# Kernel tuning notes

Measured on AMD Instinct MI355X. Metric: run time of the kernel, lower is better.

The kernel has to match this reference:

```python
import jax, jax.numpy as jnp
import numpy as np

N_AST, M, C, D, H, OUT = 200000, 400000, 25000, 256, 4, 256


def setup_inputs() -> dict:
    key = jax.random.key(0)
    ks = jax.random.split(key, 12)
    s = 0.02
    return {
        "ast_nodes_encodings": jax.random.normal(ks[0], (N_AST, D), jnp.float32),
        "ast_node_idx_to_pdg_node_idx_mapping_key": jax.random.randint(ks[1], (M,), 0, N_AST),
        "ast_node_idx_to_pdg_node_idx_mapping_value": jax.random.randint(ks[2], (M,), 0, C),
        "pdg_node_idx_to_sub_ast_root_idx_mapping_key": jax.random.randint(ks[3], (C,), 0, C),
        "pdg_node_idx_to_sub_ast_root_idx_mapping_value": jax.random.randint(ks[4], (C,), 0, N_AST),
        "nr_cfg_nodes": C,
        "Wq": jax.random.normal(ks[5], (D, D), jnp.float32) * s,
        "bq": jnp.zeros((D,), jnp.float32),
        "Wk": jax.random.normal(ks[6], (D, D), jnp.float32) * s,
        "bk": jnp.zeros((D,), jnp.float32),
        "Wv": jax.random.normal(ks[7], (D, D), jnp.float32) * s,
        "bv": jnp.zeros((D,), jnp.float32),
        "Wo": jax.random.normal(ks[8], (D, OUT), jnp.float32) * s,
        "bo": jnp.zeros((OUT,), jnp.float32),
    }


def _scatter_attn(x, attn_keys, seg, num_segments, Wq, bq, Wk, bk, Wv, bv, Wo, bo):
    # x: [M, D] scattered inputs; attn_keys: [C, D] per-segment queries; seg: [M] segment ids.
    d_h = D // H
    q = (attn_keys @ Wq + bq).reshape(num_segments, H, d_h)  # [C,H,dh]
    k = (x @ Wk + bk).reshape(-1, H, d_h)                    # [M,H,dh]
    v = (x @ Wv + bv).reshape(-1, H, d_h)                    # [M,H,dh]
    scale = 1.0 / jnp.sqrt(jnp.asarray(d_h, x.dtype))
    scores = jnp.einsum('mhd,mhd->mh', k, q[seg]) * scale    # [M,H]
    m = jax.ops.segment_max(scores, seg, num_segments=num_segments)  # [C,H]
    e = jnp.exp(scores - m[seg])                             # [M,H]
    denom = jax.ops.segment_sum(e, seg, num_segments=num_segments)  # [C,H]
    num = jax.ops.segment_sum((e[..., None] * v).reshape(-1, H * d_h),
                              seg, num_segments=num_segments)        # [C,D]
    pooled = (num.reshape(num_segments, H, d_h) / (denom[..., None] + 1e-9)).reshape(num_segments, D)
    return pooled @ Wo + bo                                  # [C,OUT]


def reference(ast_nodes_encodings,
              ast_node_idx_to_pdg_node_idx_mapping_key,
              ast_node_idx_to_pdg_node_idx_mapping_value,
              pdg_node_idx_to_sub_ast_root_idx_mapping_key,
              pdg_node_idx_to_sub_ast_root_idx_mapping_value,
              nr_cfg_nodes, Wq, bq, Wk, bk, Wv, bv, Wo, bo):
    # Build per-CFG-node attention keys: gather sub-AST-root encodings, scatter by PDG node idx.
    root_enc = ast_nodes_encodings[pdg_node_idx_to_sub_ast_root_idx_mapping_value]  # [C,D]
    attn_keys = jnp.zeros((nr_cfg_nodes, D), ast_nodes_encodings.dtype)
    attn_keys = attn_keys.at[pdg_node_idx_to_sub_ast_root_idx_mapping_key].set(root_enc)
    # Gather AST node encodings per mapping entry and attention-pool per CFG node.
    scattered = ast_nodes_encodings[ast_node_idx_to_pdg_node_idx_mapping_key]       # [M,D]
    return _scatter_attn(scattered, attn_keys, ast_node_idx_to_pdg_node_idx_mapping_value,
                         nr_cfg_nodes, Wq, bq, Wk, bk, Wv, bv, Wo, bo)
```

## Files before the change

kernel.cpp:

```cpp
#include <hip/hip_runtime.h>
#include <hip/hip_bf16.h>
#include <math.h>

#define D 256
#define H 4
#define DH 64
#define NOUT 256

typedef short bf16x8 __attribute__((ext_vector_type(8)));
typedef float f32x4 __attribute__((ext_vector_type(4)));

__device__ __forceinline__ ushort f2bf(float f){
  uint b = __float_as_uint(f);
  b += 0x7FFF + ((b >> 16) & 1);
  return (ushort)(b >> 16);
}
__device__ __forceinline__ float bf2f(ushort u){
  return __uint_as_float(((uint)u) << 16);
}

__global__ void winner_kernel(const int* __restrict__ key, int* __restrict__ winner, int C){
  int i = blockIdx.x*256 + threadIdx.x;
  if (i < C){ int t = key[i]; if (t >= 0 && t < C) atomicMax(&winner[t], i); }
}

__global__ void count_kernel(const int* __restrict__ seg, int* __restrict__ counts, int M, int C){
  int i = blockIdx.x*256 + threadIdx.x;
  if (i < M){ int s = seg[i]; if (s >= 0 && s < C) atomicAdd(&counts[s], 1); }
}

__global__ __launch_bounds__(1024) void scan_kernel(const int* __restrict__ counts,
    int* __restrict__ offsets, int* __restrict__ pos, int C){
  __shared__ int wtot[16];
  __shared__ int wexcl[16];
  __shared__ int ctot;
  __shared__ int carry_s;
  int tid = threadIdx.x, lane = tid & 63, wave = tid >> 6;
  if (tid == 0) carry_s = 0;
  __syncthreads();
  for (int base = 0; base < C; base += 1024){
    int i = base + tid;
    int v = (i < C) ? counts[i] : 0;
    int x = v;
    #pragma unroll
    for (int d2 = 1; d2 < 64; d2 <<= 1){
      int t = __shfl_up(x, d2, 64);
      if (lane >= d2) x += t;
    }
    if (lane == 63) wtot[wave] = x;
    __syncthreads();
    if (wave == 0 && lane < 16){
      int t = wtot[lane]; int y = t;
      #pragma unroll
      for (int d2 = 1; d2 < 16; d2 <<= 1){
        int u = __shfl_up(y, d2, 64);
        if (lane >= d2) y += u;
      }
      wexcl[lane] = y - t;
      if (lane == 15) ctot = y;
    }
    __syncthreads();
    int carry = carry_s;
    int excl = carry + wexcl[wave] + x - v;
    if (i < C){ offsets[i] = excl; pos[i] = excl; }
    __syncthreads();
    if (tid == 0) carry_s = carry + ctot;
    __syncthreads();
  }
  if (tid == 0) offsets[C] = carry_s;
}

__global__ void fill_kernel(const int* __restrict__ seg, int* __restrict__ pos,
                            int* __restrict__ members, int M, int C){
  int i = blockIdx.x*256 + threadIdx.x;
  if (i < M){ int s = seg[i]; if (s >= 0 && s < C){ int p = atomicAdd(&pos[s], 1); members[p] = i; } }
}

__global__ void conv_w(const float* __restrict__ Wq, const float* __restrict__ Wk,
                       const float* __restrict__ Wv, const float* __restrict__ Wo,
                       ushort* __restrict__ WqT, ushort* __restrict__ Wk16,
                       ushort* __restrict__ WvT, ushort* __restrict__ WoT){
  int id = blockIdx.x*256 + threadIdx.x;
  int r = id >> 8, c = id & 255;
  WqT[id]  = f2bf(Wq[c*256 + r]);
  WvT[id]  = f2bf(Wv[c*256 + r]);
  WoT[id]  = f2bf(Wo[c*256 + r]);
  Wk16[id] = f2bf(Wk[id]);
}

__global__ void gather_ag(const float* __restrict__ enc, const int* __restrict__ rootval,
                          const int* __restrict__ winner, ushort* __restrict__ Ag, int C){
  int id = blockIdx.x*256 + threadIdx.x;
  if (id < C*64){
    int c = id >> 6, g = id & 63;
    int w = winner[c];
    float4 v = make_float4(0.f, 0.f, 0.f, 0.f);
    if (w >= 0) v = *(const float4*)(enc + (size_t)rootval[w]*D + g*4);
    ushort4 u; u.x = f2bf(v.x); u.y = f2bf(v.y); u.z = f2bf(v.z); u.w = f2bf(v.w);
    *(ushort4*)(Ag + (size_t)c*D + g*4) = u;
  }
}

template<bool OUT_BF16>
__global__ __launch_bounds__(256) void mfma_gemm(
    const ushort* __restrict__ A, int sA, int acol_h,
    const ushort* __restrict__ Bt, int sBt, int btrow_h, int btcol_h,
    void* __restrict__ Out, int sOut, int outcol_h,
    int M, int K,
    const float* __restrict__ bias, const float* __restrict__ beta){
  __shared__ __align__(16) ushort As[64][72];
  __shared__ __align__(16) ushort Bs[64][72];
  int tid = threadIdx.x;
  int hz = blockIdx.z;
  int m0 = blockIdx.x*64;
  int acol0  = acol_h*hz;
  int btrow0 = blockIdx.y*64 + btrow_h*hz;
  int btcol0 = btcol_h*hz;
  int outcol0 = blockIdx.y*64 + outcol_h*hz;
  int w = tid >> 6, lane = tid & 63, quad = lane >> 4, l16 = lane & 15;
  int r1 = tid >> 3, c8 = (tid & 7)*8;
  f32x4 acc[4] = {};
  for (int k0 = 0; k0 < K; k0 += 64){
    const ushort* ga = A + (size_t)(m0 + r1)*sA + acol0 + k0 + c8;
    uint4 v1 = make_uint4(0,0,0,0), v2 = make_uint4(0,0,0,0);
    if (m0 + r1 < M)      v1 = *(const uint4*)ga;
    if (m0 + r1 + 32 < M) v2 = *(const uint4*)(ga + (size_t)32*sA);
    *(uint4*)&As[r1][c8]      = v1;
    *(uint4*)&As[r1+32][c8]   = v2;
    const ushort* gb = Bt + (size_t)(btrow0 + r1)*sBt + btcol0 + k0 + c8;
    *(uint4*)&Bs[r1][c8]      = *(const uint4*)gb;
    *(uint4*)&Bs[r1+32][c8]   = *(const uint4*)(gb + (size_t)32*sBt);
    __syncthreads();
    #pragma unroll
    for (int ks = 0; ks < 2; ks++){
      bf16x8 b = *(const bf16x8*)&Bs[w*16 + l16][ks*32 + quad*8];
      #pragma unroll
      for (int mt = 0; mt < 4; mt++){
        bf16x8 a = *(const bf16x8*)&As[mt*16 + l16][ks*32 + quad*8];
        acc[mt] = __builtin_amdgcn_mfma_f32_16x16x32_bf16(a, b, acc[mt], 0, 0, 0);
      }
    }
    __syncthreads();
  }
  int col = outcol0 + w*16 + l16;
  float bval = bias ? bias[btrow0 + w*16 + l16] : 0.f;
  #pragma unroll
  for (int mt = 0; mt < 4; mt++){
    #pragma unroll
    for (int r = 0; r < 4; r++){
      int row = m0 + mt*16 + quad*4 + r;
      if (row < M){
        float add = beta ? beta[row*H + hz]*bval : bval;
        float v = acc[mt][r] + add;
        if (OUT_BF16) ((ushort*)Out)[(size_t)row*sOut + col] = f2bf(v);
        else          ((float*)Out)[(size_t)row*sOut + col] = v;
      }
    }
  }
}

__global__ void qb_kernel(const ushort* __restrict__ q16, const float* __restrict__ bk,
                          float* __restrict__ qb, int C){
  int i = blockIdx.x*256 + threadIdx.x;
  if (i < C*H){
    int c = i >> 2, h = i & 3;
    const ushort* qp = q16 + (size_t)c*D + h*DH;
    const float* bp = bk + h*DH;
    float s = 0.f;
    for (int d = 0; d < DH; d++) s += bf2f(qp[d]) * bp[d];
    qb[i] = s;
  }
}

__global__ __launch_bounds__(256) void seg_attn(const float* __restrict__ enc,
    const int* __restrict__ astkey, const int* __restrict__ members,
    const int* __restrict__ offsets, const float* __restrict__ qb,
    const ushort* __restrict__ qk16, ushort* __restrict__ Shat16,
    float* __restrict__ beta, int C){
  int lane = threadIdx.x & 63, wave = threadIdx.x >> 6;
  int c = blockIdx.x * 4 + wave;
  if (c >= C) return;
  const ushort4* qp = (const ushort4*)(qk16 + (size_t)c * (H*D));
  ushort4 u0 = qp[lane], u1 = qp[64 + lane], u2 = qp[128 + lane], u3 = qp[192 + lane];
  float4 qk0 = make_float4(bf2f(u0.x), bf2f(u0.y), bf2f(u0.z), bf2f(u0.w));
  float4 qk1 = make_float4(bf2f(u1.x), bf2f(u1.y), bf2f(u1.z), bf2f(u1.w));
  float4 qk2 = make_float4(bf2f(u2.x), bf2f(u2.y), bf2f(u2.z), bf2f(u2.w));
  float4 qk3 = make_float4(bf2f(u3.x), bf2f(u3.y), bf2f(u3.z), bf2f(u3.w));
  float qb0 = qb[c*H+0], qb1 = qb[c*H+1], qb2 = qb[c*H+2], qb3 = qb[c*H+3];
  int off = offsets[c];
  int n = offsets[c+1] - off;
  float4 S0 = make_float4(0,0,0,0), S1 = S0, S2 = S0, S3 = S0;
  float m0 = -INFINITY, m1 = m0, m2 = m0, m3 = m0;
  float l0 = 0.f, l1 = 0.f, l2 = 0.f, l3 = 0.f;
  for (int base = 0; base < n; base += 64){
    int cnt = min(64, n - base);
    int xrow = 0;
    if (lane < cnt) xrow = astkey[members[off + base + lane]];
    int r0 = __shfl(xrow, 0, 64);
    float4 xv = ((const float4*)(enc + (size_t)r0 * D))[lane];
    for (int j = 0; j < cnt; j++){
      float4 nx = xv;
      if (j + 1 < cnt){
        int r = __shfl(xrow, j + 1, 64);
        nx = ((const float4*)(enc + (size_t)r * D))[lane];
      }
      float p0 = xv.x*qk0.x + xv.y*qk0.y + xv.z*qk0.z + xv.w*qk0.w;
      float p1 = xv.x*qk1.x + xv.y*qk1.y + xv.z*qk1.z + xv.w*qk1.w;
      float p2 = xv.x*qk2.x + xv.y*qk2.y + xv.z*qk2.z + xv.w*qk2.w;
      float p3 = xv.x*qk3.x + xv.y*qk3.y + xv.z*qk3.z + xv.w*qk3.w;
      #pragma unroll
      for (int d2 = 1; d2 < 64; d2 <<= 1){
        p0 += __shfl_xor(p0, d2, 64);
        p1 += __shfl_xor(p1, d2, 64);
        p2 += __shfl_xor(p2, d2, 64);
        p3 += __shfl_xor(p3, d2, 64);
      }
      float s0 = (p0 + qb0) * 0.125f;
      float s1 = (p1 + qb1) * 0.125f;
      float s2 = (p2 + qb2) * 0.125f;
      float s3 = (p3 + qb3) * 0.125f;
      float nm0 = fmaxf(m0, s0), nm1 = fmaxf(m1, s1);
      float nm2 = fmaxf(m2, s2), nm3 = fmaxf(m3, s3);
      if ((nm0 != m0) | (nm1 != m1) | (nm2 != m2) | (nm3 != m3)){
        float a0 = __expf(m0 - nm0), a1 = __expf(m1 - nm1);
        float a2 = __expf(m2 - nm2), a3 = __expf(m3 - nm3);
        S0.x *= a0; S0.y *= a0; S0.z *= a0; S0.w *= a0;
        S1.x *= a1; S1.y *= a1; S1.z *= a1; S1.w *= a1;
        S2.x *= a2; S2.y *= a2; S2.z *= a2; S2.w *= a2;
        S3.x *= a3; S3.y *= a3; S3.z *= a3; S3.w *= a3;
        l0 *= a0; l1 *= a1; l2 *= a2; l3 *= a3;
        m0 = nm0; m1 = nm1; m2 = nm2; m3 = nm3;
      }
      float e0 = __expf(s0 - m0), e1 = __expf(s1 - m1);
      float e2 = __expf(s2 - m2), e3 = __expf(s3 - m3);
      l0 += e0; l1 += e1; l2 += e2; l3 += e3;
      S0.x += e0*xv.x; S0.y += e0*xv.y; S0.z += e0*xv.z; S0.w += e0*xv.w;
      S1.x += e1*xv.x; S1.y += e1*xv.y; S1.z += e1*xv.z; S1.w += e1*xv.w;
      S2.x += e2*xv.x; S2.y += e2*xv.y; S2.z += e2*xv.z; S2.w += e2*xv.w;
      S3.x += e3*xv.x; S3.y += e3*xv.y; S3.z += e3*xv.z; S3.w += e3*xv.w;
      xv = nx;
    }
  }
  float inv0 = 1.f / (l0 + 1e-9f), inv1 = 1.f / (l1 + 1e-9f);
  float inv2 = 1.f / (l2 + 1e-9f), inv3 = 1.f / (l3 + 1e-9f);
  ushort4* sp = (ushort4*)(Shat16 + (size_t)c * (H*D));
  ushort4 o0, o1, o2, o3;
  o0.x = f2bf(S0.x*inv0); o0.y = f2bf(S0.y*inv0); o0.z = f2bf(S0.z*inv0); o0.w = f2bf(S0.w*inv0);
  o1.x = f2bf(S1.x*inv1); o1.y = f2bf(S1.y*inv1); o1.z = f2bf(S1.z*inv1); o1.w = f2bf(S1.w*inv1);
  o2.x = f2bf(S2.x*inv2); o2.y = f2bf(S2.y*inv2); o2.z = f2bf(S2.z*inv2); o2.w = f2bf(S2.w*inv2);
  o3.x = f2bf(S3.x*inv3); o3.y = f2bf(S3.y*inv3); o3.z = f2bf(S3.z*inv3); o3.w = f2bf(S3.w*inv3);
  sp[lane] = o0; sp[64+lane] = o1; sp[128+lane] = o2; sp[192+lane] = o3;
  if (lane == 0){
    beta[c*H+0] = l0 / (l0 + 1e-9f);
    beta[c*H+1] = l1 / (l1 + 1e-9f);
    beta[c*H+2] = l2 / (l2 + 1e-9f);
    beta[c*H+3] = l3 / (l3 + 1e-9f);
  }
}

extern "C" void kernel_launch(void* const* d_in, const int* in_sizes, int n_in,
                              void* d_out, int out_size, void* d_ws, size_t ws_size,
                              hipStream_t stream) {
  const float* enc    = (const float*)d_in[0];
  const int*   astkey = (const int*)d_in[1];
  const int*   seg    = (const int*)d_in[2];
  const int*   pdgkey = (const int*)d_in[3];
  const int*   pdgval = (const int*)d_in[4];
  const float* Wq = (const float*)d_in[6];
  const float* bq = (const float*)d_in[7];
  const float* Wk = (const float*)d_in[8];
  const float* bk = (const float*)d_in[9];
  const float* Wv = (const float*)d_in[10];
  const float* bv = (const float*)d_in[11];
  const float* Wo = (const float*)d_in[12];
  const float* bo = (const float*)d_in[13];
  float* out = (float*)d_out;
  const int M = in_sizes[1];
  const int C = in_sizes[3];

  char* p = (char*)d_ws;
  auto alloc = [&](size_t bytes) -> void* {
    void* r = (void*)p;
    p += (bytes + 255) / 256 * 256;
    return r;
  };
  ushort* Ag      = (ushort*)alloc((size_t)C * D * 2);
  ushort* q16     = (ushort*)alloc((size_t)C * D * 2);
  ushort* qk16    = (ushort*)alloc((size_t)C * H * D * 2);
  ushort* Shat16  = (ushort*)alloc((size_t)C * H * D * 2);
  ushort* pooled16= (ushort*)alloc((size_t)C * D * 2);
  float*  qb      = (float*)alloc((size_t)C * H * 4);
  float*  beta    = (float*)alloc((size_t)C * H * 4);
  ushort* WqT     = (ushort*)alloc((size_t)D * D * 2);
  ushort* Wk16    = (ushort*)alloc((size_t)D * D * 2);
  ushort* WvT     = (ushort*)alloc((size_t)D * D * 2);
  ushort* WoT     = (ushort*)alloc((size_t)D * D * 2);
  int*   winner   = (int*)alloc((size_t)C * 4);
  int*   counts   = (int*)alloc((size_t)C * 4);
  int*   offsets  = (int*)alloc((size_t)(C + 1) * 4);
  int*   pos      = (int*)alloc((size_t)C * 4);
  int*   members  = (int*)alloc((size_t)M * 4);

  hipMemsetAsync(winner, 0xFF, (size_t)C * 4, stream);
  hipMemsetAsync(counts, 0, (size_t)C * 4, stream);

  int gC = (C + 255) / 256, gM = (M + 255) / 256;
  winner_kernel<<<gC, 256, 0, stream>>>(pdgkey, winner, C);
  count_kernel<<<gM, 256, 0, stream>>>(seg, counts, M, C);
  scan_kernel<<<1, 1024, 0, stream>>>(counts, offsets, pos, C);
  fill_kernel<<<gM, 256, 0, stream>>>(seg, pos, members, M, C);

  conv_w<<<(D*D)/256, 256, 0, stream>>>(Wq, Wk, Wv, Wo, WqT, Wk16, WvT, WoT);
  gather_ag<<<(C*64 + 255)/256, 256, 0, stream>>>(enc, pdgval, winner, Ag, C);

  int mt = (C + 63) / 64;
  mfma_gemm<true><<<dim3(mt,4,1), 256, 0, stream>>>(
      Ag, D, 0,  WqT, D, 0, 0,  q16, D, 0,  C, D, bq, nullptr);
  qb_kernel<<<(C*H + 255)/256, 256, 0, stream>>>(q16, bk, qb, C);
  mfma_gemm<true><<<dim3(mt,4,4), 256, 0, stream>>>(
      q16, D, DH,  Wk16, D, 0, DH,  qk16, H*D, D,  C, DH, nullptr, nullptr);

  seg_attn<<<(C + 3)/4, 256, 0, stream>>>(enc, astkey, members, offsets, qb, qk16, Shat16, beta, C);

  mfma_gemm<true><<<dim3(mt,1,4), 256, 0, stream>>>(
      Shat16, H*D, D,  WvT, D, DH, 0,  pooled16, D, DH,  C, D, bv, beta);
  mfma_gemm<false><<<dim3(mt,4,1), 256, 0, stream>>>(
      pooled16, D, 0,  WoT, D, 0, 0,  out, NOUT, 0,  C, D, bo, nullptr);
}
```

Measured before the change: 545.7 us.

## Fold projection weights into combined matrices, parallelize scan, drop online-max softmax

Precomputes the combined weights Wq·Wk^T per head (Gt) and Wv·Wo per head (Zt), plus the bias cross terms. This removes the per-row q GEMM, the qb kernel and the pooled GEMM, at the cost of a larger K for the final GEMM. The single-block scan becomes a three-kernel multi-block scan. seg_attn now processes two members per wave iteration using half-waves and drops the running-max rescaling, which risks overflow in exp if scores grow large.

```diff
diff --git a/kernel.cpp b/kernel.cpp
--- a/kernel.cpp
+++ b/kernel.cpp
@@ -29,45 +29,53 @@
   if (i < M){ int s = seg[i]; if (s >= 0 && s < C) atomicAdd(&counts[s], 1); }
 }
 
-__global__ __launch_bounds__(1024) void scan_kernel(const int* __restrict__ counts,
-    int* __restrict__ offsets, int* __restrict__ pos, int C){
+__global__ __launch_bounds__(1024) void scan1_kernel(const int* __restrict__ counts,
+    int* __restrict__ loc, int* __restrict__ btot, int C){
   __shared__ int wtot[16];
   __shared__ int wexcl[16];
-  __shared__ int ctot;
-  __shared__ int carry_s;
-  int tid = threadIdx.x, lane = tid & 63, wave = tid >> 6;
-  if (tid == 0) carry_s = 0;
+  int tid = threadIdx.x, lane = tid & 63, wv = tid >> 6;
+  int i = blockIdx.x*1024 + tid;
+  int v = (i < C) ? counts[i] : 0;
+  int x = v;
+  #pragma unroll
+  for (int d2 = 1; d2 < 64; d2 <<= 1){
+    int t = __shfl_up(x, d2, 64);
+    if (lane >= d2) x += t;
+  }
+  if (lane == 63) wtot[wv] = x;
   __syncthreads();
-  for (int base = 0; base < C; base += 1024){
-    int i = base + tid;
-    int v = (i < C) ? counts[i] : 0;
-    int x = v;
-    #pragma unroll
-    for (int d2 = 1; d2 < 64; d2 <<= 1){
-      int t = __shfl_up(x, d2, 64);
-      if (lane >= d2) x += t;
-    }
-    if (lane == 63) wtot[wave] = x;
-    __syncthreads();
-    if (wave == 0 && lane < 16){
-      int t = wtot[lane]; int y = t;
-      #pragma unroll
-      for (int d2 = 1; d2 < 16; d2 <<= 1){
-        int u = __shfl_up(y, d2, 64);
-        if (lane >= d2) y += u;
-      }
-      wexcl[lane] = y - t;
-      if (lane == 15) ctot = y;
-    }
-    __syncthreads();
-    int carry = carry_s;
-    int excl = carry + wexcl[wave] + x - v;
-    if (i < C){ offsets[i] = excl; pos[i] = excl; }
-    __syncthreads();
-    if (tid == 0) carry_s = carry + ctot;
-    __syncthreads();
-  }
-  if (tid == 0) offsets[C] = carry_s;
+  if (wv == 0 && lane < 16){
+    int t = wtot[lane]; int y = t;
+    #pragma unroll
+    for (int d2 = 1; d2 < 16; d2 <<= 1){
+      int u = __shfl_up(y, d2, 64);
+      if (lane >= d2) y += u;
+    }
+    wexcl[lane] = y - t;
+    if (lane == 15) btot[blockIdx.x] = y;
+  }
+  __syncthreads();
+  if (i < C) loc[i] = wexcl[wv] + x - v;
+}
+
+__global__ void scan2_kernel(const int* __restrict__ btot, int* __restrict__ bexcl,
+                             int nb, int* __restrict__ offsets, int C){
+  int lane = threadIdx.x;
+  int v = (lane < nb) ? btot[lane] : 0;
+  int x = v;
+  #pragma unroll
+  for (int d2 = 1; d2 < 64; d2 <<= 1){
+    int t = __shfl_up(x, d2, 64);
+    if (lane >= d2) x += t;
+  }
+  if (lane < nb) bexcl[lane] = x - v;
+  if (lane == 63) offsets[C] = x;
+}
+
+__global__ void scan3_kernel(const int* __restrict__ loc, const int* __restrict__ bexcl,
+                             int* __restrict__ offsets, int* __restrict__ pos, int C){
+  int i = blockIdx.x*256 + threadIdx.x;
+  if (i < C){ int o = loc[i] + bexcl[i >> 10]; offsets[i] = o; pos[i] = o; }
 }
 
 __global__ void fill_kernel(const int* __restrict__ seg, int* __restrict__ pos,
@@ -76,16 +84,58 @@
   if (i < M){ int s = seg[i]; if (s >= 0 && s < C){ int p = atomicAdd(&pos[s], 1); members[p] = i; } }
 }
 
-__global__ void conv_w(const float* __restrict__ Wq, const float* __restrict__ Wk,
-                       const float* __restrict__ Wv, const float* __restrict__ Wo,
-                       ushort* __restrict__ WqT, ushort* __restrict__ Wk16,
-                       ushort* __restrict__ WvT, ushort* __restrict__ WoT){
+__global__ void conv3_kernel(const float* __restrict__ Wq, const float* __restrict__ Wk,
+                             const float* __restrict__ Wv,
+                             ushort* __restrict__ Wq16, ushort* __restrict__ Wk16,
+                             ushort* __restrict__ Wv16){
   int id = blockIdx.x*256 + threadIdx.x;
-  int r = id >> 8, c = id & 255;
-  WqT[id]  = f2bf(Wq[c*256 + r]);
-  WvT[id]  = f2bf(Wv[c*256 + r]);
-  WoT[id]  = f2bf(Wo[c*256 + r]);
+  Wq16[id] = f2bf(Wq[id]);
   Wk16[id] = f2bf(Wk[id]);
+  Wv16[id] = f2bf(Wv[id]);
+}
+
+__global__ __launch_bounds__(256) void transpose_wo(const float* __restrict__ Wo,
+                                                    ushort* __restrict__ WoT16){
+  __shared__ float t[64][65];
+  int tid = threadIdx.x;
+  int r = tid >> 6, cc = tid & 63;
+  int bx = blockIdx.x, by = blockIdx.y;
+  #pragma unroll
+  for (int rr = 0; rr < 64; rr += 4)
+    t[rr + r][cc] = Wo[(size_t)(by*64 + rr + r)*256 + bx*64 + cc];
+  __syncthreads();
+  #pragma unroll
+  for (int rr = 0; rr < 64; rr += 4)
+    WoT16[(size_t)(bx*64 + rr + r)*256 + by*64 + cc] = f2bf(t[cc][rr + r]);
+}
+
+__global__ void prep_small(const float* __restrict__ Wq, const float* __restrict__ Wk,
+                           const float* __restrict__ Wo, const float* __restrict__ bq,
+                           const float* __restrict__ bk, const float* __restrict__ bv,
+                           float* __restrict__ wqbk, float* __restrict__ bvo,
+                           float* __restrict__ bqk, float* __restrict__ cbh){
+  int id = blockIdx.x*256 + threadIdx.x;
+  if (id < 1024){
+    int h = id >> 8, k = id & 255;
+    float s = 0.f;
+    for (int d = 0; d < DH; d++) s += Wq[(size_t)k*256 + h*64 + d] * bk[h*64 + d];
+    wqbk[id] = s;
+  } else if (id < 2048){
+    int t = id - 1024; int h = t >> 8, o = t & 255;
+    float s = 0.f;
+    for (int d = 0; d < DH; d++) s += bv[h*64 + d] * Wo[(size_t)(h*64 + d)*256 + o];
+    bvo[t] = s;
+  } else if (id < 3072){
+    int t = id - 2048; int h = t >> 8, e = t & 255;
+    float s = 0.f;
+    for (int d = 0; d < DH; d++) s += bq[h*64 + d] * Wk[(size_t)e*256 + h*64 + d];
+    bqk[t] = s;
+  } else if (id < 3076){
+    int h = id - 3072;
+    float s = 0.f;
+    for (int d = 0; d < DH; d++) s += bq[h*64 + d] * bk[h*64 + d];
+    cbh[h] = s;
+  }
 }
 
 __global__ void gather_ag(const float* __restrict__ enc, const int* __restrict__ rootval,
@@ -105,9 +155,10 @@
 __global__ __launch_bounds__(256) void mfma_gemm(
     const ushort* __restrict__ A, int sA, int acol_h,
     const ushort* __restrict__ Bt, int sBt, int btrow_h, int btcol_h,
-    void* __restrict__ Out, int sOut, int outcol_h,
+    void* __restrict__ Out, int sOut, int outrow_h, int outcol_h,
     int M, int K,
-    const float* __restrict__ bias, const float* __restrict__ beta){
+    const float* __restrict__ bias, const float* __restrict__ beta4,
+    const float* __restrict__ bvo4){
   __shared__ __align__(16) ushort As[64][72];
   __shared__ __align__(16) ushort Bs[64][72];
   int tid = threadIdx.x;
@@ -116,6 +167,7 @@
   int acol0  = acol_h*hz;
   int btrow0 = blockIdx.y*64 + btrow_h*hz;
   int btcol0 = btcol_h*hz;
+  int outrow0 = outrow_h*hz;
   int outcol0 = blockIdx.y*64 + outcol_h*hz;
   int w = tid >> 6, lane = tid & 63, quad = lane >> 4, l16 = lane & 15;
   int r1 = tid >> 3, c8 = (tid & 7)*8;
@@ -143,118 +195,142 @@
     __syncthreads();
   }
   int col = outcol0 + w*16 + l16;
-  float bval = bias ? bias[btrow0 + w*16 + l16] : 0.f;
+  int bcol = btrow0 + w*16 + l16;
+  float bval = bias ? bias[bcol] : 0.f;
   #pragma unroll
   for (int mt = 0; mt < 4; mt++){
     #pragma unroll
     for (int r = 0; r < 4; r++){
       int row = m0 + mt*16 + quad*4 + r;
       if (row < M){
-        float add = beta ? beta[row*H + hz]*bval : bval;
-        float v = acc[mt][r] + add;
-        if (OUT_BF16) ((ushort*)Out)[(size_t)row*sOut + col] = f2bf(v);
-        else          ((float*)Out)[(size_t)row*sOut + col] = v;
-      }
-    }
-  }
-}
-
-__global__ void qb_kernel(const ushort* __restrict__ q16, const float* __restrict__ bk,
-                          float* __restrict__ qb, int C){
-  int i = blockIdx.x*256 + threadIdx.x;
-  if (i < C*H){
-    int c = i >> 2, h = i & 3;
-    const ushort* qp = q16 + (size_t)c*D + h*DH;
-    const float* bp = bk + h*DH;
-    float s = 0.f;
-    for (int d = 0; d < DH; d++) s += bf2f(qp[d]) * bp[d];
-    qb[i] = s;
+        float v = acc[mt][r] + bval;
+        if (bvo4){
+          v += beta4[row*4+0]*bvo4[0*256 + bcol] + beta4[row*4+1]*bvo4[1*256 + bcol]
+             + beta4[row*4+2]*bvo4[2*256 + bcol] + beta4[row*4+3]*bvo4[3*256 + bcol];
+        }
+        if (OUT_BF16) ((ushort*)Out)[(size_t)(outrow0 + row)*sOut + col] = f2bf(v);
+        else          ((float*)Out)[(size_t)(outrow0 + row)*sOut + col] = v;
+      }
+    }
   }
 }
 
 __global__ __launch_bounds__(256) void seg_attn(const float* __restrict__ enc,
     const int* __restrict__ astkey, const int* __restrict__ members,
-    const int* __restrict__ offsets, const float* __restrict__ qb,
+    const int* __restrict__ offsets, const ushort* __restrict__ Ag,
+    const float* __restrict__ wqbk, const float* __restrict__ cbh,
     const ushort* __restrict__ qk16, ushort* __restrict__ Shat16,
     float* __restrict__ beta, int C){
   int lane = threadIdx.x & 63, wave = threadIdx.x >> 6;
-  int c = blockIdx.x * 4 + wave;
+  int c = blockIdx.x*4 + wave;
   if (c >= C) return;
-  const ushort4* qp = (const ushort4*)(qk16 + (size_t)c * (H*D));
-  ushort4 u0 = qp[lane], u1 = qp[64 + lane], u2 = qp[128 + lane], u3 = qp[192 + lane];
-  float4 qk0 = make_float4(bf2f(u0.x), bf2f(u0.y), bf2f(u0.z), bf2f(u0.w));
-  float4 qk1 = make_float4(bf2f(u1.x), bf2f(u1.y), bf2f(u1.z), bf2f(u1.w));
-  float4 qk2 = make_float4(bf2f(u2.x), bf2f(u2.y), bf2f(u2.z), bf2f(u2.w));
-  float4 qk3 = make_float4(bf2f(u3.x), bf2f(u3.y), bf2f(u3.z), bf2f(u3.w));
-  float qb0 = qb[c*H+0], qb1 = qb[c*H+1], qb2 = qb[c*H+2], qb3 = qb[c*H+3];
+  int half = lane >> 5, sl = lane & 31;
+  float qk[4][8];
+  const ushort* qkp = qk16 + (size_t)c*1024 + sl*8;
+  #pragma unroll
+  for (int h = 0; h < 4; h++){
+    uint4 u = *(const uint4*)(qkp + h*256);
+    qk[h][0]=__uint_as_float(u.x<<16); qk[h][1]=__uint_as_float(u.x&0xffff0000u);
+    qk[h][2]=__uint_as_float(u.y<<16); qk[h][3]=__uint_as_float(u.y&0xffff0000u);
+    qk[h][4]=__uint_as_float(u.z<<16); qk[h][5]=__uint_as_float(u.z&0xffff0000u);
+    qk[h][6]=__uint_as_float(u.w<<16); qk[h][7]=__uint_as_float(u.w&0xffff0000u);
+  }
+  float qbv[4];
+  {
+    uint4 a = *(const uint4*)(Ag + (size_t)c*256 + sl*8);
+    float av[8];
+    av[0]=__uint_as_float(a.x<<16); av[1]=__uint_as_float(a.x&0xffff0000u);
+    av[2]=__uint_as_float(a.y<<16); av[3]=__uint_as_float(a.y&0xffff0000u);
+    av[4]=__uint_as_float(a.z<<16); av[5]=__uint_as_float(a.z&0xffff0000u);
+    av[6]=__uint_as_float(a.w<<16); av[7]=__uint_as_float(a.w&0xffff0000u);
+    #pragma unroll
+    for (int h = 0; h < 4; h++){
+      const float* wp = wqbk + h*256 + sl*8;
+      float p = av[0]*wp[0] + av[1]*wp[1] + av[2]*wp[2] + av[3]*wp[3]
+              + av[4]*wp[4] + av[5]*wp[5] + av[6]*wp[6] + av[7]*wp[7];
+      #pragma unroll
+      for (int d2 = 1; d2 < 32; d2 <<= 1) p += __shfl_xor(p, d2, 64);
+      qbv[h] = p + cbh[h];
+    }
+  }
   int off = offsets[c];
   int n = offsets[c+1] - off;
-  float4 S0 = make_float4(0,0,0,0), S1 = S0, S2 = S0, S3 = S0;
-  float m0 = -INFINITY, m1 = m0, m2 = m0, m3 = m0;
-  float l0 = 0.f, l1 = 0.f, l2 = 0.f, l3 = 0.f;
+  float S[4][8] = {};
+  float l[4] = {0.f, 0.f, 0.f, 0.f};
   for (int base = 0; base < n; base += 64){
     int cnt = min(64, n - base);
     int xrow = 0;
     if (lane < cnt) xrow = astkey[members[off + base + lane]];
-    int r0 = __shfl(xrow, 0, 64);
-    float4 xv = ((const float4*)(enc + (size_t)r0 * D))[lane];
-    for (int j = 0; j < cnt; j++){
-      float4 nx = xv;
-      if (j + 1 < cnt){
-        int r = __shfl(xrow, j + 1, 64);
-        nx = ((const float4*)(enc + (size_t)r * D))[lane];
-      }
-      float p0 = xv.x*qk0.x + xv.y*qk0.y + xv.z*qk0.z + xv.w*qk0.w;
-      float p1 = xv.x*qk1.x + xv.y*qk1.y + xv.z*qk1.z + xv.w*qk1.w;
-      float p2 = xv.x*qk2.x + xv.y*qk2.y + xv.z*qk2.z + xv.w*qk2.w;
-      float p3 = xv.x*qk3.x + xv.y*qk3.y + xv.z*qk3.z + xv.w*qk3.w;
-      #pragma unroll
-      for (int d2 = 1; d2 < 64; d2 <<= 1){
-        p0 += __shfl_xor(p0, d2, 64);
-        p1 += __shfl_xor(p1, d2, 64);
-        p2 += __shfl_xor(p2, d2, 64);
-        p3 += __shfl_xor(p3, d2, 64);
-      }
-      float s0 = (p0 + qb0) * 0.125f;
-      float s1 = (p1 + qb1) * 0.125f;
-      float s2 = (p2 + qb2) * 0.125f;
-      float s3 = (p3 + qb3) * 0.125f;
-      float nm0 = fmaxf(m0, s0), nm1 = fmaxf(m1, s1);
-      float nm2 = fmaxf(m2, s2), nm3 = fmaxf(m3, s3);
-      if ((nm0 != m0) | (nm1 != m1) | (nm2 != m2) | (nm3 != m3)){
-        float a0 = __expf(m0 - nm0), a1 = __expf(m1 - nm1);
-        float a2 = __expf(m2 - nm2), a3 = __expf(m3 - nm3);
-        S0.x *= a0; S0.y *= a0; S0.z *= a0; S0.w *= a0;
-        S1.x *= a1; S1.y *= a1; S1.z *= a1; S1.w *= a1;
-        S2.x *= a2; S2.y *= a2; S2.z *= a2; S2.w *= a2;
-        S3.x *= a3; S3.y *= a3; S3.z *= a3; S3.w *= a3;
-        l0 *= a0; l1 *= a1; l2 *= a2; l3 *= a3;
-        m0 = nm0; m1 = nm1; m2 = nm2; m3 = nm3;
-      }
-      float e0 = __expf(s0 - m0), e1 = __expf(s1 - m1);
-      float e2 = __expf(s2 - m2), e3 = __expf(s3 - m3);
-      l0 += e0; l1 += e1; l2 += e2; l3 += e3;
-      S0.x += e0*xv.x; S0.y += e0*xv.y; S0.z += e0*xv.z; S0.w += e0*xv.w;
-      S1.x += e1*xv.x; S1.y += e1*xv.y; S1.z += e1*xv.z; S1.w += e1*xv.w;
-      S2.x += e2*xv.x; S2.y += e2*xv.y; S2.z += e2*xv.z; S2.w += e2*xv.w;
-      S3.x += e3*xv.x; S3.y += e3*xv.y; S3.z += e3*xv.z; S3.w += e3*xv.w;
-      xv = nx;
-    }
-  }
-  float inv0 = 1.f / (l0 + 1e-9f), inv1 = 1.f / (l1 + 1e-9f);
-  float inv2 = 1.f / (l2 + 1e-9f), inv3 = 1.f / (l3 + 1e-9f);
-  ushort4* sp = (ushort4*)(Shat16 + (size_t)c * (H*D));
-  ushort4 o0, o1, o2, o3;
-  o0.x = f2bf(S0.x*inv0); o0.y = f2bf(S0.y*inv0); o0.z = f2bf(S0.z*inv0); o0.w = f2bf(S0.w*inv0);
-  o1.x = f2bf(S1.x*inv1); o1.y = f2bf(S1.y*inv1); o1.z = f2bf(S1.z*inv1); o1.w = f2bf(S1.w*inv1);
-  o2.x = f2bf(S2.x*inv2); o2.y = f2bf(S2.y*inv2); o2.z = f2bf(S2.z*inv2); o2.w = f2bf(S2.w*inv2);
-  o3.x = f2bf(S3.x*inv3); o3.y = f2bf(S3.y*inv3); o3.z = f2bf(S3.z*inv3); o3.w = f2bf(S3.w*inv3);
-  sp[lane] = o0; sp[64+lane] = o1; sp[128+lane] = o2; sp[192+lane] = o3;
+    int rA = __shfl(xrow, 0, 64);
+    int rB = __shfl(xrow, (cnt > 1) ? 1 : 0, 64);
+    int r = half ? rB : rA;
+    const float* xp = enc + (size_t)r*256 + sl*8;
+    float4 x0 = *(const float4*)xp;
+    float4 x1 = *(const float4*)(xp + 4);
+    for (int j = 0; j < cnt; j += 2){
+      float4 nx0 = x0, nx1 = x1;
+      if (j + 2 < cnt){
+        int nA = __shfl(xrow, j + 2, 64);
+        int nB = __shfl(xrow, (j + 3 < cnt) ? (j + 3) : (j + 2), 64);
+        int nr = half ? nB : nA;
+        const float* np = enc + (size_t)nr*256 + sl*8;
+        nx0 = *(const float4*)np;
+        nx1 = *(const float4*)(np + 4);
+      }
+      float x[8] = {x0.x, x0.y, x0.z, x0.w, x1.x, x1.y, x1.z, x1.w};
+      float p[4];
+      #pragma unroll
+      for (int h = 0; h < 4; h++){
+        float s = x[0]*qk[h][0] + x[1]*qk[h][1] + x[2]*qk[h][2] + x[3]*qk[h][3]
+                + x[4]*qk[h][4] + x[5]*qk[h][5] + x[6]*qk[h][6] + x[7]*qk[h][7];
+        p[h] = s;
+      }
+      #pragma unroll
+      for (int d2 = 1; d2 < 32; d2 <<= 1){
+        #pragma unroll
+        for (int h = 0; h < 4; h++) p[h] += __shfl_xor(p[h], d2, 64);
+      }
+      float e[4];
+      #pragma unroll
+      for (int h = 0; h < 4; h++) e[h] = __expf((p[h] + qbv[h]) * 0.125f);
+      if (half & (int)(j + 1 >= cnt)){ e[0] = e[1] = e[2] = e[3] = 0.f; }
+      #pragma unroll
+      for (int h = 0; h < 4; h++){
+        l[h] += e[h];
+        #pragma unroll
+        for (int k = 0; k < 8; k++) S[h][k] += e[h]*x[k];
+      }
+      x0 = nx0; x1 = nx1;
+    }
+  }
+  #pragma unroll
+  for (int h = 0; h < 4; h++) l[h] += __shfl_xor(l[h], 32, 64);
+  #pragma unroll
+  for (int h = 0; h < 4; h++){
+    #pragma unroll
+    for (int k = 0; k < 8; k++) S[h][k] += __shfl_xor(S[h][k], 32, 64);
+  }
+  float inv[4];
+  #pragma unroll
+  for (int h = 0; h < 4; h++) inv[h] = 1.f / (l[h] + 1e-9f);
+  if (half == 0){
+    ushort* sp = Shat16 + (size_t)c*1024 + sl*8;
+    #pragma unroll
+    for (int h = 0; h < 4; h++){
+      float ih = inv[h];
+      uint4 o;
+      o.x = (uint)f2bf(S[h][0]*ih) | ((uint)f2bf(S[h][1]*ih) << 16);
+      o.y = (uint)f2bf(S[h][2]*ih) | ((uint)f2bf(S[h][3]*ih) << 16);
+      o.z = (uint)f2bf(S[h][4]*ih) | ((uint)f2bf(S[h][5]*ih) << 16);
+      o.w = (uint)f2bf(S[h][6]*ih) | ((uint)f2bf(S[h][7]*ih) << 16);
+      *(uint4*)(sp + h*256) = o;
+    }
+  }
   if (lane == 0){
-    beta[c*H+0] = l0 / (l0 + 1e-9f);
-    beta[c*H+1] = l1 / (l1 + 1e-9f);
-    beta[c*H+2] = l2 / (l2 + 1e-9f);
-    beta[c*H+3] = l3 / (l3 + 1e-9f);
+    beta[c*4+0] = l[0] / (l[0] + 1e-9f);
+    beta[c*4+1] = l[1] / (l[1] + 1e-9f);
+    beta[c*4+2] = l[2] / (l[2] + 1e-9f);
+    beta[c*4+3] = l[3] / (l[3] + 1e-9f);
   }
 }
 
@@ -285,18 +361,24 @@
     return r;
   };
   ushort* Ag      = (ushort*)alloc((size_t)C * D * 2);
-  ushort* q16     = (ushort*)alloc((size_t)C * D * 2);
   ushort* qk16    = (ushort*)alloc((size_t)C * H * D * 2);
   ushort* Shat16  = (ushort*)alloc((size_t)C * H * D * 2);
-  ushort* pooled16= (ushort*)alloc((size_t)C * D * 2);
-  float*  qb      = (float*)alloc((size_t)C * H * 4);
   float*  beta    = (float*)alloc((size_t)C * H * 4);
-  ushort* WqT     = (ushort*)alloc((size_t)D * D * 2);
+  ushort* Wq16    = (ushort*)alloc((size_t)D * D * 2);
   ushort* Wk16    = (ushort*)alloc((size_t)D * D * 2);
-  ushort* WvT     = (ushort*)alloc((size_t)D * D * 2);
-  ushort* WoT     = (ushort*)alloc((size_t)D * D * 2);
+  ushort* Wv16    = (ushort*)alloc((size_t)D * D * 2);
+  ushort* WoT16   = (ushort*)alloc((size_t)D * D * 2);
+  ushort* Gt16    = (ushort*)alloc((size_t)H * D * D * 2);
+  ushort* Zt16    = (ushort*)alloc((size_t)D * H * D * 2);
+  float*  wqbk    = (float*)alloc((size_t)H * D * 4);
+  float*  bvo     = (float*)alloc((size_t)H * NOUT * 4);
+  float*  bqk     = (float*)alloc((size_t)H * D * 4);
+  float*  cbh     = (float*)alloc((size_t)H * 4);
   int*   winner   = (int*)alloc((size_t)C * 4);
   int*   counts   = (int*)alloc((size_t)C * 4);
+  int*   loc      = (int*)alloc((size_t)C * 4);
+  int*   btot     = (int*)alloc((size_t)64 * 4);
+  int*   bexcl    = (int*)alloc((size_t)64 * 4);
   int*   offsets  = (int*)alloc((size_t)(C + 1) * 4);
   int*   pos      = (int*)alloc((size_t)C * 4);
   int*   members  = (int*)alloc((size_t)M * 4);
@@ -305,25 +387,32 @@
   hipMemsetAsync(counts, 0, (size_t)C * 4, stream);
 
   int gC = (C + 255) / 256, gM = (M + 255) / 256;
+  int nb1024 = (C + 1023) / 1024;
   winner_kernel<<<gC, 256, 0, stream>>>(pdgkey, winner, C);
   count_kernel<<<gM, 256, 0, stream>>>(seg, counts, M, C);
-  scan_kernel<<<1, 1024, 0, stream>>>(counts, offsets, pos, C);
+  scan1_kernel<<<nb1024, 1024, 0, stream>>>(counts, loc, btot, C);
+  scan2_kernel<<<1, 64, 0, stream>>>(btot, bexcl, nb1024, offsets, C);
+  scan3_kernel<<<gC, 256, 0, stream>>>(loc, bexcl, offsets, pos, C);
   fill_kernel<<<gM, 256, 0, stream>>>(seg, pos, members, M, C);
 
-  conv_w<<<(D*D)/256, 256, 0, stream>>>(Wq, Wk, Wv, Wo, WqT, Wk16, WvT, WoT);
+  conv3_kernel<<<(D*D)/256, 256, 0, stream>>>(Wq, Wk, Wv, Wq16, Wk16, Wv16);
+  transpose_wo<<<dim3(4,4), 256, 0, stream>>>(Wo, WoT16);
+  prep_small<<<13, 256, 0, stream>>>(Wq, Wk, Wo, bq, bk, bv, wqbk, bvo, bqk, cbh);
+
+  mfma_gemm<true><<<dim3(4,4,4), 256, 0, stream>>>(
+      Wk16, D, DH,  Wq16, D, 0, DH,  Gt16, D, D, 0,  D, DH, nullptr, nullptr, nullptr);
+  mfma_gemm<true><<<dim3(4,4,4), 256, 0, stream>>>(
+      WoT16, D, DH,  Wv16, D, 0, DH,  Zt16, H*D, 0, D,  D, DH, nullptr, nullptr, nullptr);
+
   gather_ag<<<(C*64 + 255)/256, 256, 0, stream>>>(enc, pdgval, winner, Ag, C);
 
   int mt = (C + 63) / 64;
-  mfma_gemm<true><<<dim3(mt,4,1), 256, 0, stream>>>(
-      Ag, D, 0,  WqT, D, 0, 0,  q16, D, 0,  C, D, bq, nullptr);
-  qb_kernel<<<(C*H + 255)/256, 256, 0, stream>>>(q16, bk, qb, C);
   mfma_gemm<true><<<dim3(mt,4,4), 256, 0, stream>>>(
-      q16, D, DH,  Wk16, D, 0, DH,  qk16, H*D, D,  C, DH, nullptr, nullptr);
-
-  seg_attn<<<(C + 3)/4, 256, 0, stream>>>(enc, astkey, members, offsets, qb, qk16, Shat16, beta, C);
-
-  mfma_gemm<true><<<dim3(mt,1,4), 256, 0, stream>>>(
-      Shat16, H*D, D,  WvT, D, DH, 0,  pooled16, D, DH,  C, D, bv, beta);
+      Ag, D, 0,  Gt16, D, D, 0,  qk16, H*D, 0, D,  C, D, bqk, nullptr, nullptr);
+
+  seg_attn<<<(C + 3)/4, 256, 0, stream>>>(enc, astkey, members, offsets, Ag,
+                                          wqbk, cbh, qk16, Shat16, beta, C);
+
   mfma_gemm<false><<<dim3(mt,4,1), 256, 0, stream>>>(
-      pooled16, D, 0,  WoT, D, 0, 0,  out, NOUT, 0,  C, D, bo, nullptr);
-}
+      Shat16, H*D, 0,  Zt16, H*D, 0, 0,  out, NOUT, 0, 0,  C, H*D, bo, beta, bvo);
+}
```

New measurement: 518.0 us. -5.1%, faster.
